# Kernel optimization log

Hardware: AMD Instinct MI355X
Metric: run time of the kernel (lower is better)

Reference implementation:

```python
import jax, jax.numpy as jnp
import numpy as np

B, IN, OUT, G = 64, 8192, 8192, 64
NG = IN // G  # groups per row


def setup_inputs() -> dict:
    key = jax.random.key(0)
    k1, k2, k3, k4 = jax.random.split(key, 4)
    x = jax.random.normal(k1, (B, IN), dtype=jnp.float32)
    # packed 2-bit codes: 4 codes per byte, LSB-first (matches _pack2)
    w_packed = jax.random.randint(k2, (OUT, IN // 4), 0, 256, dtype=jnp.int32).astype(jnp.uint8)
    # scales from _calc_group_qparams are positive (max_abs/1.5); zp is always 2
    scales = jax.random.uniform(k3, (OUT, NG), dtype=jnp.float32, minval=0.01, maxval=0.1)
    zps = jnp.full((OUT, NG), 2, dtype=jnp.int32)
    bias = jax.random.normal(k4, (OUT,), dtype=jnp.float32) * 0.01
    return {"x": x, "w_packed": w_packed, "scales": scales, "zps": zps, "bias": bias}


def _dequant(w_packed, scales, zps):
    # unpack: byte -> 4 two-bit codes, LSB first (matches _unpack2)
    out_f = w_packed.shape[0]
    codes = jnp.stack([(w_packed >> s) & 3 for s in (0, 2, 4, 6)], axis=-1)  # [OUT, IN//4, 4]
    q = codes.reshape(out_f, NG, G).astype(jnp.int32)                        # [OUT, NG, G]
    # per-group dequant: (q - zp) * scale
    w = (q - zps[:, :, None]).astype(jnp.float32) * scales[:, :, None]
    return w.reshape(out_f, IN)                                              # [OUT, IN]


def reference(x, w_packed, scales, zps, bias):
    w = _dequant(w_packed, scales, zps)  # [OUT, IN] fp32
    # original accumulates xg @ wg.T per group; equivalent to full x @ w.T
    return x @ w.T + bias                # [B, OUT]
```

## Files before the change

kernel.cpp:

```cpp
#include <hip/hip_runtime.h>
#include <hip/hip_bf16.h>

#define B_    64
#define IN_   8192
#define OUT_  8192
#define NG_   128
#define PB_   2048
#define KSPLIT 16
#define KC    512

typedef float    f32x16 __attribute__((ext_vector_type(16)));
typedef short    s16x8  __attribute__((ext_vector_type(8)));
typedef _Float16 f16x4  __attribute__((ext_vector_type(4)));

#define OFF_WQ   (1u << 20)
#define OFF_SQ   (17u << 20)
#define OFF_ZF   (19u << 20)
#define OFF_PART (20u << 20)

__global__ __launch_bounds__(256) void k_prep(
    const float* __restrict__ x, const unsigned char* __restrict__ wp,
    const float* __restrict__ scales, const int* __restrict__ zps,
    uint4* __restrict__ xfrag, unsigned char* __restrict__ wq,
    uint4* __restrict__ sq, int* __restrict__ zflags)
{
    __shared__ uint4 lds[2048];
    __shared__ int zf;
    const int bid = blockIdx.x, tid = threadIdx.x;

    if (bid < 512) {
        const unsigned v = ((const unsigned*)wp)[tid];
        const bool u8mode = __any((int)(v > 255u));
        if (u8mode) {
            const uint4* src = (const uint4*)wp + bid * 2048;
#pragma unroll
            for (int i = 0; i < 8; ++i) lds[tid + i * 256] = src[tid + i * 256];
        } else {
            const int* src = (const int*)wp + bid * 32768;
#pragma unroll
            for (int i = 0; i < 8; ++i) {
                const int j = tid + i * 256;
                const int* p = src + j * 16;
                unsigned d[4];
#pragma unroll
                for (int w = 0; w < 4; ++w)
                    d[w] = (unsigned)(p[w*4] & 0xFF) | ((unsigned)(p[w*4+1] & 0xFF) << 8) |
                           ((unsigned)(p[w*4+2] & 0xFF) << 16) | ((unsigned)(p[w*4+3] & 0xFF) << 24);
                lds[j] = (uint4){d[0], d[1], d[2], d[3]};
            }
        }
        __syncthreads();
        const int c = tid >> 4, r = tid & 15;
        uint4* dst = (uint4*)wq + ((unsigned)c * OUT_ + bid * 16 + r) * 8;
#pragma unroll
        for (int u = 0; u < 8; ++u) dst[u] = lds[r * 128 + c * 8 + u];
    } else if (bid < 576) {
        const int b2 = bid - 512;
        const int kidx = b2 >> 2, prt = b2 & 3;
#pragma unroll
        for (int i = 0; i < 4; ++i) {
            const int idx = prt * 1024 + i * 256 + tid;
            const int sg = idx >> 6, lane = idx & 63;
            const int t = sg >> 1, mt = sg & 1;
            const int h = lane >> 5, m = lane & 31;
            const float* src = x + (mt * 32 + m) * IN_ + kidx * KC + h * 256 + t * 8;
            const float4 f0 = *(const float4*)src;
            const float4 f1 = *(const float4*)(src + 4);
            __hip_bfloat162 h0 = __float22bfloat162_rn(make_float2(f0.x, f0.y));
            __hip_bfloat162 h1 = __float22bfloat162_rn(make_float2(f0.z, f0.w));
            __hip_bfloat162 h2 = __float22bfloat162_rn(make_float2(f1.x, f1.y));
            __hip_bfloat162 h3 = __float22bfloat162_rn(make_float2(f1.z, f1.w));
            uint4 o;
            o.x = *(unsigned*)&h0; o.y = *(unsigned*)&h1;
            o.z = *(unsigned*)&h2; o.w = *(unsigned*)&h3;
            xfrag[kidx * 4096 + idx] = o;
        }
    } else {
        const int b3 = bid - 576;
        if (tid < 128) {
            const int n = b3 * 128 + tid;
#pragma unroll
            for (int kidx = 0; kidx < 16; ++kidx) {
                const float* sp = scales + n * NG_ + kidx * 8;
                const float4 s0 = *(const float4*)sp;
                const float4 s1 = *(const float4*)(sp + 4);
                __hip_bfloat162 h0 = __float22bfloat162_rn(make_float2(s0.x, s0.y));
                __hip_bfloat162 h1 = __float22bfloat162_rn(make_float2(s0.z, s0.w));
                __hip_bfloat162 h2 = __float22bfloat162_rn(make_float2(s1.x, s1.y));
                __hip_bfloat162 h3 = __float22bfloat162_rn(make_float2(s1.z, s1.w));
                uint4 o;
                o.x = *(unsigned*)&h0; o.y = *(unsigned*)&h1;
                o.z = *(unsigned*)&h2; o.w = *(unsigned*)&h3;
                sq[(unsigned)kidx * OUT_ + n] = o;
            }
        }
        if (tid == 0) zf = 0;
        __syncthreads();
        int bad = 0;
        const int4* zp4 = (const int4*)zps + b3 * 4096;
#pragma unroll
        for (int i = 0; i < 16; ++i) {
            const int4 z = zp4[i * 256 + tid];
            bad |= (z.x != 2) | (z.y != 2) | (z.z != 2) | (z.w != 2);
        }
        if (bad) zf = 1;
        __syncthreads();
        if (tid == 0) zflags[b3] = zf;
    }
}

__global__ __launch_bounds__(256, 2) void k_main(
    const uint4* __restrict__ xfrag, const unsigned char* __restrict__ wq,
    const uint2* __restrict__ sq2, const int* __restrict__ zflags,
    const int* __restrict__ zps, _Float16* __restrict__ part)
{
    __shared__ uint4 x_lds[4096];

    const int tid = threadIdx.x, wave = tid >> 6, lane = tid & 63;
    const int h = lane >> 5, n32 = lane & 31;
    const int kidx = blockIdx.x & (KSPLIT - 1);
    const int nblk = blockIdx.x >> 4;
    const int colbase = nblk * 256 + wave * 64;

    uint4 w[2][4];
    uint2 sv[2];
    int ncol[2];
#pragma unroll
    for (int cg = 0; cg < 2; ++cg) {
        const int n = colbase + cg * 32 + n32;
        ncol[cg] = n;
        const uint4* wb = (const uint4*)(wq + ((unsigned)kidx * OUT_ + n) * 128 + h * 64);
        w[cg][0] = wb[0];
        w[cg][1] = wb[1];
        sv[cg] = sq2[((unsigned)kidx * OUT_ + n) * 2 + h];
    }
    const int zv = zflags[lane & 63];
#pragma unroll
    for (int i = 0; i < 8; ++i) {
        const int sg = wave * 8 + i;
        const uint4* src = xfrag + kidx * 4096 + sg * 64 + lane;
        __builtin_amdgcn_global_load_lds(
            (const __attribute__((address_space(1))) unsigned*)src,
            (__attribute__((address_space(3))) unsigned*)((char*)x_lds + sg * 1024),
            16, 0, 0);
    }
    const bool zgen = __any(zv != 0);
    __syncthreads();

#pragma unroll
    for (int cg = 0; cg < 2; ++cg) {
        const uint4* wb = (const uint4*)(wq + ((unsigned)kidx * OUT_ + ncol[cg]) * 128 + h * 64);
        w[cg][2] = wb[2];
        w[cg][3] = wb[3];
    }
#pragma unroll
    for (int i = 0; i < 8; ++i) {
        const int sg = 32 + wave * 8 + i;
        const uint4* src = xfrag + kidx * 4096 + sg * 64 + lane;
        __builtin_amdgcn_global_load_lds(
            (const __attribute__((address_space(1))) unsigned*)src,
            (__attribute__((address_space(3))) unsigned*)((char*)x_lds + sg * 1024),
            16, 0, 0);
    }

    unsigned tl[2][4], th[2][4];
#pragma unroll
    for (int cg = 0; cg < 2; ++cg) {
#pragma unroll
        for (int gg = 0; gg < 4; ++gg) {
            const unsigned dwv = (gg >> 1) ? sv[cg].y : sv[cg].x;
            const unsigned s16 = (gg & 1) ? (dwv >> 16) : (dwv & 0xFFFFu);
            if (!zgen) {
                const unsigned m1 = s16 | 0x8000u;
                const unsigned m2 = (s16 + 0x0080u) | 0x8000u;
                tl[cg][gg] = m2 | (m1 << 16);
                th[cg][gg] = s16 << 16;
            } else {
                union { unsigned u; float f; } sf; sf.u = s16 << 16;
                const int g = kidx * 8 + h * 4 + gg;
                const float zf = (float)zps[ncol[cg] * NG_ + g];
                const float v0 = (0.f - zf) * sf.f, v1 = (1.f - zf) * sf.f;
                const float v2 = (2.f - zf) * sf.f, v3 = (3.f - zf) * sf.f;
                __hip_bfloat162 lo = __float22bfloat162_rn(make_float2(v0, v1));
                __hip_bfloat162 hi = __float22bfloat162_rn(make_float2(v2, v3));
                tl[cg][gg] = *(unsigned*)&lo;
                th[cg][gg] = *(unsigned*)&hi;
            }
        }
    }

    f32x16 acc[2][2];
#pragma unroll
    for (int cg = 0; cg < 2; ++cg)
#pragma unroll
        for (int mt = 0; mt < 2; ++mt)
#pragma unroll
            for (int r = 0; r < 16; ++r) acc[cg][mt][r] = 0.f;

#pragma unroll
    for (int p = 0; p < 2; ++p) {
        if (p) __syncthreads();
#pragma unroll
        for (int t8 = 0; t8 < 2; ++t8) {
#pragma unroll
            for (int dw = 0; dw < 4; ++dw) {
#pragma unroll
                for (int hf = 0; hf < 2; ++hf) {
                    const int t = p * 16 + t8 * 8 + dw * 2 + hf;
                    union { uint4 u4; s16x8 s8; } av[2];
#pragma unroll
                    for (int mt = 0; mt < 2; ++mt)
                        av[mt].u4 = x_lds[(t * 2 + mt) * 64 + lane];
#pragma unroll
                    for (int cg = 0; cg < 2; ++cg) {
                        const uint4 wc = w[cg][p * 2 + t8];
                        const unsigned wdw = ((const unsigned*)&wc)[dw];
                        const unsigned u = hf ? (wdw >> 16) : (wdw & 0xFFFFu);
                        const unsigned tlv = tl[cg][p * 2 + t8];
                        const unsigned thv = th[cg][p * 2 + t8];
                        union { unsigned w_[4]; s16x8 s8; } bf;
#pragma unroll
                        for (int m = 0; m < 4; ++m) {
                            const unsigned c0 = (u >> (4 * m)) & 3u;
                            const unsigned c1 = (u >> (4 * m + 2)) & 3u;
                            const unsigned sel = 0x01000100u + c0 * 0x0202u + c1 * 0x02020000u;
                            bf.w_[m] = __builtin_amdgcn_perm(thv, tlv, sel);
                        }
#pragma unroll
                        for (int mt = 0; mt < 2; ++mt)
                            acc[cg][mt] = __builtin_amdgcn_mfma_f32_32x32x16_bf16(
                                av[mt].s8, bf.s8, acc[cg][mt], 0, 0, 0);
                    }
                }
            }
        }
    }

    _Float16* pp = part + kidx * (B_ * OUT_);
#pragma unroll
    for (int cg = 0; cg < 2; ++cg) {
        const int col = ncol[cg];
#pragma unroll
        for (int mt = 0; mt < 2; ++mt)
#pragma unroll
            for (int r = 0; r < 16; ++r) {
                const int row = (r & 3) + 8 * (r >> 2) + 4 * h;
                pp[(mt * 32 + row) * OUT_ + col] = (_Float16)acc[cg][mt][r];
            }
    }
}

__global__ __launch_bounds__(256) void k_reduce(const _Float16* __restrict__ part,
                                                const float* __restrict__ bias,
                                                float* __restrict__ out) {
    const int gtid = blockIdx.x * 256 + threadIdx.x;
    const int b  = gtid >> 11;
    const int n0 = (gtid & 2047) * 4;
    float4 s = *(const float4*)(bias + n0);
#pragma unroll
    for (int p = 0; p < KSPLIT; ++p) {
        const f16x4 v = *(const f16x4*)(part + p * (B_ * OUT_) + b * OUT_ + n0);
        s.x += (float)v[0]; s.y += (float)v[1];
        s.z += (float)v[2]; s.w += (float)v[3];
    }
    *(float4*)(out + b * OUT_ + n0) = s;
}

extern "C" void kernel_launch(void* const* d_in, const int* in_sizes, int n_in,
                              void* d_out, int out_size, void* d_ws, size_t ws_size,
                              hipStream_t stream) {
    const float*         x      = (const float*)d_in[0];
    const unsigned char* wp     = (const unsigned char*)d_in[1];
    const float*         scales = (const float*)d_in[2];
    const int*           zps    = (const int*)d_in[3];
    const float*         bias   = (const float*)d_in[4];
    float*               out    = (float*)d_out;

    char* ws = (char*)d_ws;
    uint4*         xfrag = (uint4*)ws;
    unsigned char* wq    = (unsigned char*)(ws + OFF_WQ);
    uint4*         sq    = (uint4*)(ws + OFF_SQ);
    int*           zfl   = (int*)(ws + OFF_ZF);
    _Float16*      part  = (_Float16*)(ws + OFF_PART);

    k_prep<<<640, 256, 0, stream>>>(x, wp, scales, zps, xfrag, wq, sq, zfl);
    k_main<<<512, 256, 0, stream>>>(xfrag, wq, (const uint2*)sq, zfl, zps, part);
    k_reduce<<<512, 256, 0, stream>>>(part, bias, out);
}
```

Baseline: 132.9 us.

## Drop LDS staging in weight prep and pipeline weight loads in main loop

The prep kernel's weight repack now goes straight through registers, with each thread reading its own row chunk and writing to the transposed layout. This removes the LDS buffer and the block barrier. The main kernel now issues all x fragment loads into LDS at once with a single barrier. Weight loads are double-buffered: the next 16-byte chunk is fetched while the current one is used in MFMAs, replacing the earlier split of two loads before and two after the barrier. This trades explicit overlap of x loads with compute for fewer barriers and streamed weight prefetch, and the uncoalesced direct global reads in prep may cost bandwidth.

```diff
diff --git a/kernel.cpp b/kernel.cpp
--- a/kernel.cpp
+++ b/kernel.cpp
@@ -24,36 +24,35 @@
     uint4* __restrict__ xfrag, unsigned char* __restrict__ wq,
     uint4* __restrict__ sq, int* __restrict__ zflags)
 {
-    __shared__ uint4 lds[2048];
     __shared__ int zf;
     const int bid = blockIdx.x, tid = threadIdx.x;
 
     if (bid < 512) {
+        const int c = tid & 15, r = tid >> 4;
         const unsigned v = ((const unsigned*)wp)[tid];
         const bool u8mode = __any((int)(v > 255u));
+        uint4 buf[8];
         if (u8mode) {
-            const uint4* src = (const uint4*)wp + bid * 2048;
-#pragma unroll
-            for (int i = 0; i < 8; ++i) lds[tid + i * 256] = src[tid + i * 256];
+            const uint4* src = (const uint4*)(wp + (bid * 16 + r) * PB_ + c * 128);
+#pragma unroll
+            for (int u = 0; u < 8; ++u) buf[u] = src[u];
         } else {
-            const int* src = (const int*)wp + bid * 32768;
-#pragma unroll
-            for (int i = 0; i < 8; ++i) {
-                const int j = tid + i * 256;
-                const int* p = src + j * 16;
+            const int* src = (const int*)wp + (bid * 16 + r) * PB_ + c * 128;
+#pragma unroll
+            for (int u = 0; u < 8; ++u) {
                 unsigned d[4];
 #pragma unroll
-                for (int w = 0; w < 4; ++w)
-                    d[w] = (unsigned)(p[w*4] & 0xFF) | ((unsigned)(p[w*4+1] & 0xFF) << 8) |
-                           ((unsigned)(p[w*4+2] & 0xFF) << 16) | ((unsigned)(p[w*4+3] & 0xFF) << 24);
-                lds[j] = (uint4){d[0], d[1], d[2], d[3]};
-            }
-        }
-        __syncthreads();
-        const int c = tid >> 4, r = tid & 15;
-        uint4* dst = (uint4*)wq + ((unsigned)c * OUT_ + bid * 16 + r) * 8;
-#pragma unroll
-        for (int u = 0; u < 8; ++u) dst[u] = lds[r * 128 + c * 8 + u];
+                for (int w = 0; w < 4; ++w) {
+                    const int* p = src + u * 16 + w * 4;
+                    d[w] = (unsigned)(p[0] & 0xFF) | ((unsigned)(p[1] & 0xFF) << 8) |
+                           ((unsigned)(p[2] & 0xFF) << 16) | ((unsigned)(p[3] & 0xFF) << 24);
+                }
+                buf[u] = (uint4){d[0], d[1], d[2], d[3]};
+            }
+        }
+        uint4* dst = (uint4*)(wq + ((unsigned)c * OUT_ + bid * 16 + r) * 128);
+#pragma unroll
+        for (int u = 0; u < 8; ++u) dst[u] = buf[u];
     } else if (bid < 576) {
         const int b2 = bid - 512;
         const int kidx = b2 >> 2, prt = b2 & 3;
@@ -122,22 +121,18 @@
     const int nblk = blockIdx.x >> 4;
     const int colbase = nblk * 256 + wave * 64;
 
-    uint4 w[2][4];
+    int ncol[2];
     uint2 sv[2];
-    int ncol[2];
 #pragma unroll
     for (int cg = 0; cg < 2; ++cg) {
-        const int n = colbase + cg * 32 + n32;
-        ncol[cg] = n;
-        const uint4* wb = (const uint4*)(wq + ((unsigned)kidx * OUT_ + n) * 128 + h * 64);
-        w[cg][0] = wb[0];
-        w[cg][1] = wb[1];
-        sv[cg] = sq2[((unsigned)kidx * OUT_ + n) * 2 + h];
-    }
-    const int zv = zflags[lane & 63];
-#pragma unroll
-    for (int i = 0; i < 8; ++i) {
-        const int sg = wave * 8 + i;
+        ncol[cg] = colbase + cg * 32 + n32;
+        sv[cg] = sq2[((unsigned)kidx * OUT_ + ncol[cg]) * 2 + h];
+    }
+    const int zv = zflags[lane];
+
+#pragma unroll
+    for (int i = 0; i < 16; ++i) {
+        const int sg = wave * 16 + i;
         const uint4* src = xfrag + kidx * 4096 + sg * 64 + lane;
         __builtin_amdgcn_global_load_lds(
             (const __attribute__((address_space(1))) unsigned*)src,
@@ -146,22 +141,7 @@
     }
     const bool zgen = __any(zv != 0);
     __syncthreads();
-
-#pragma unroll
-    for (int cg = 0; cg < 2; ++cg) {
-        const uint4* wb = (const uint4*)(wq + ((unsigned)kidx * OUT_ + ncol[cg]) * 128 + h * 64);
-        w[cg][2] = wb[2];
-        w[cg][3] = wb[3];
-    }
-#pragma unroll
-    for (int i = 0; i < 8; ++i) {
-        const int sg = 32 + wave * 8 + i;
-        const uint4* src = xfrag + kidx * 4096 + sg * 64 + lane;
-        __builtin_amdgcn_global_load_lds(
-            (const __attribute__((address_space(1))) unsigned*)src,
-            (__attribute__((address_space(3))) unsigned*)((char*)x_lds + sg * 1024),
-            16, 0, 0);
-    }
+    __builtin_amdgcn_sched_barrier(0);
 
     unsigned tl[2][4], th[2][4];
 #pragma unroll
@@ -197,43 +177,44 @@
 #pragma unroll
             for (int r = 0; r < 16; ++r) acc[cg][mt][r] = 0.f;
 
-#pragma unroll
-    for (int p = 0; p < 2; ++p) {
-        if (p) __syncthreads();
-#pragma unroll
-        for (int t8 = 0; t8 < 2; ++t8) {
-#pragma unroll
-            for (int dw = 0; dw < 4; ++dw) {
-#pragma unroll
-                for (int hf = 0; hf < 2; ++hf) {
-                    const int t = p * 16 + t8 * 8 + dw * 2 + hf;
-                    union { uint4 u4; s16x8 s8; } av[2];
+    const uint4* wb0 = (const uint4*)(wq + ((unsigned)kidx * OUT_ + ncol[0]) * 128 + h * 64);
+    const uint4* wb1 = (const uint4*)(wq + ((unsigned)kidx * OUT_ + ncol[1]) * 128 + h * 64);
+    uint4 wcur0 = wb0[0], wcur1 = wb1[0];
+#pragma unroll
+    for (int c = 0; c < 4; ++c) {
+        uint4 wn0, wn1;
+        if (c < 3) { wn0 = wb0[c + 1]; wn1 = wb1[c + 1]; }
+#pragma unroll
+        for (int dw = 0; dw < 4; ++dw) {
+#pragma unroll
+            for (int hf = 0; hf < 2; ++hf) {
+                const int t = c * 8 + dw * 2 + hf;
+                union { uint4 u4; s16x8 s8; } av[2];
+#pragma unroll
+                for (int mt = 0; mt < 2; ++mt)
+                    av[mt].u4 = x_lds[(t * 2 + mt) * 64 + lane];
+#pragma unroll
+                for (int cg = 0; cg < 2; ++cg) {
+                    const uint4 wc = cg ? wcur1 : wcur0;
+                    const unsigned wdw = ((const unsigned*)&wc)[dw];
+                    const unsigned u = hf ? (wdw >> 16) : (wdw & 0xFFFFu);
+                    const unsigned tlv = tl[cg][c], thv = th[cg][c];
+                    union { unsigned w_[4]; s16x8 s8; } bf;
+#pragma unroll
+                    for (int m = 0; m < 4; ++m) {
+                        const unsigned c0 = (u >> (4 * m)) & 3u;
+                        const unsigned c1 = (u >> (4 * m + 2)) & 3u;
+                        const unsigned sel = 0x01000100u + c0 * 0x0202u + c1 * 0x02020000u;
+                        bf.w_[m] = __builtin_amdgcn_perm(thv, tlv, sel);
+                    }
 #pragma unroll
                     for (int mt = 0; mt < 2; ++mt)
-                        av[mt].u4 = x_lds[(t * 2 + mt) * 64 + lane];
-#pragma unroll
-                    for (int cg = 0; cg < 2; ++cg) {
-                        const uint4 wc = w[cg][p * 2 + t8];
-                        const unsigned wdw = ((const unsigned*)&wc)[dw];
-                        const unsigned u = hf ? (wdw >> 16) : (wdw & 0xFFFFu);
-                        const unsigned tlv = tl[cg][p * 2 + t8];
-                        const unsigned thv = th[cg][p * 2 + t8];
-                        union { unsigned w_[4]; s16x8 s8; } bf;
-#pragma unroll
-                        for (int m = 0; m < 4; ++m) {
-                            const unsigned c0 = (u >> (4 * m)) & 3u;
-                            const unsigned c1 = (u >> (4 * m + 2)) & 3u;
-                            const unsigned sel = 0x01000100u + c0 * 0x0202u + c1 * 0x02020000u;
-                            bf.w_[m] = __builtin_amdgcn_perm(thv, tlv, sel);
-                        }
-#pragma unroll
-                        for (int mt = 0; mt < 2; ++mt)
-                            acc[cg][mt] = __builtin_amdgcn_mfma_f32_32x32x16_bf16(
-                                av[mt].s8, bf.s8, acc[cg][mt], 0, 0, 0);
-                    }
+                        acc[cg][mt] = __builtin_amdgcn_mfma_f32_32x32x16_bf16(
+                            av[mt].s8, bf.s8, acc[cg][mt], 0, 0, 0);
                 }
             }
         }
+        if (c < 3) { wcur0 = wn0; wcur1 = wn1; }
     }
 
     _Float16* pp = part + kidx * (B_ * OUT_);
```

Measured after the change: 137.6 us. 1.04x slower.
